# Optimization experiments

Hardware: AMD Instinct MI355X
Metric: run time of the kernel (lower is better)

## Reference

```python
import jax, jax.numpy as jnp
import numpy as np

D = 4096  # uniform layer width (sizes[i])
L = 4     # number of MyLinear layers (maximum)


def setup_inputs() -> dict:
    key = jax.random.key(0)
    ks = jax.random.split(key, 8)
    x = jax.random.normal(ks[0], (D,), jnp.float32)
    W_in = jax.random.normal(ks[1], (D, D), jnp.float32) / np.float32(np.sqrt(D))
    b_in = jax.random.normal(ks[2], (D,), jnp.float32) * 0.01
    weights = jax.random.normal(ks[3], (L, D, D), jnp.float32) / np.float32(np.sqrt(D))
    # `order` is a fixed 0/1-style connectivity mask (requires_grad=False in torch)
    orders = (jax.random.uniform(ks[4], (L, D, D)) < 0.5).astype(jnp.float32)
    biases = jax.random.normal(ks[5], (L, D), jnp.float32) * 0.01
    # input_layer[i]: which node slots feed layer i (irregular gather)
    gather_idx = jax.random.randint(ks[6], (L, D), 0, D)
    # layer_nodes[k]: where layer outputs are scattered (per-layer permutation)
    scatter_idx = jnp.stack(
        [jax.random.permutation(jax.random.fold_in(ks[7], i), D) for i in range(L + 1)]
    )
    return dict(x=x, W_in=W_in, b_in=b_in, weights=weights, orders=orders,
                biases=biases, gather_idx=gather_idx, scatter_idx=scatter_idx)


def reference(x, W_in, b_in, weights, orders, biases, gather_idx, scatter_idx):
    # input layer: relu(Linear(x)), scattered into the node buffer
    out0 = jax.nn.relu(W_in @ x + b_in)              # [D]
    buf = jnp.zeros_like(out0).at[scatter_idx[0]].set(out0)

    def step(buf, layer):
        W, O, b, g, s = layer
        inp = buf[g]                                  # gather node values [D]
        out = jax.nn.relu((W * O) @ inp + b)          # masked GEMV + bias + relu
        new_buf = jnp.zeros_like(out).at[s].set(out)  # scatter into node buffer
        return new_buf, out

    _, outs = jax.lax.scan(
        step, buf, (weights, orders, biases, gather_idx, scatter_idx[1:])
    )
    return outs[-1]  # forward returns the last layer's (pre-scatter) output
```

## Files before the change

kernel.cpp:

```cpp
#include <hip/hip_runtime.h>
#include <hip/hip_bf16.h>


#define DD 4096
#define BLOCK 512
#define GRID  512

template<bool MASKED>
__global__ __launch_bounds__(BLOCK)
void gemv_kernel(const float* __restrict__ W,
                 const float* __restrict__ O,
                 const float* __restrict__ bias,
                 const float* __restrict__ src,
                 const int*   __restrict__ g,
                 const int*   __restrict__ s,
                 float*       __restrict__ dst)
{
    __shared__ float sh[DD];
    const int tid = threadIdx.x;

    #pragma unroll
    for (int j = tid; j < DD; j += BLOCK)
        sh[j] = MASKED ? src[g[j]] : src[j];
    __syncthreads();

    const int lane = tid & 63;
    const int wv   = tid >> 6;
    const int row  = blockIdx.x * 8 + wv;

    const float* __restrict__ Wr = W + (size_t)row * DD + lane * 4;
    const float* __restrict__ Or = MASKED ? (O + (size_t)row * DD + lane * 4)
                                          : nullptr;

    float4 w[16];
    #pragma unroll
    for (int it = 0; it < 16; ++it)
        w[it] = *reinterpret_cast<const float4*>(Wr + it * 256);

    float4 o[16];
    if (MASKED) {
        #pragma unroll
        for (int it = 0; it < 16; ++it)
            o[it] = *reinterpret_cast<const float4*>(Or + it * 256);
    }

    float a0 = 0.f, a1 = 0.f, a2 = 0.f, a3 = 0.f;
    #pragma unroll
    for (int it = 0; it < 16; ++it) {
        float4 v = *reinterpret_cast<const float4*>(sh + it * 256 + lane * 4);
        float4 ww = w[it];
        if (MASKED) {
            ww.x *= o[it].x; ww.y *= o[it].y; ww.z *= o[it].z; ww.w *= o[it].w;
        }
        a0 = fmaf(ww.x, v.x, a0);
        a1 = fmaf(ww.y, v.y, a1);
        a2 = fmaf(ww.z, v.z, a2);
        a3 = fmaf(ww.w, v.w, a3);
    }
    float acc = (a0 + a1) + (a2 + a3);

    #pragma unroll
    for (int off = 32; off > 0; off >>= 1)
        acc += __shfl_xor(acc, off, 64);

    if (lane == 0) {
        float r = fmaxf(acc + bias[row], 0.f);
        if (s) dst[s[row]] = r;
        else   dst[row]    = r;
    }
}

extern "C" void kernel_launch(void* const* d_in, const int* in_sizes, int n_in,
                              void* d_out, int out_size, void* d_ws, size_t ws_size,
                              hipStream_t stream) {
    const float* x       = (const float*)d_in[0];
    const float* W_in    = (const float*)d_in[1];
    const float* b_in    = (const float*)d_in[2];
    const float* weights = (const float*)d_in[3];
    const float* orders  = (const float*)d_in[4];
    const float* biases  = (const float*)d_in[5];
    const int*   gidx    = (const int*)d_in[6];
    const int*   sidx    = (const int*)d_in[7];
    float*       out     = (float*)d_out;

    float* buf0 = (float*)d_ws;
    float* buf1 = buf0 + DD;

    gemv_kernel<false><<<GRID, BLOCK, 0, stream>>>(
        W_in, nullptr, b_in, x, nullptr, sidx, buf0);

    float* cur = buf0;
    float* nxt = buf1;
    for (int l = 0; l < 4; ++l) {
        const int* s  = (l == 3) ? nullptr : (sidx + (size_t)(l + 1) * DD);
        float*     d  = (l == 3) ? out     : nxt;
        gemv_kernel<true><<<GRID, BLOCK, 0, stream>>>(
            weights + (size_t)l * DD * DD,
            orders  + (size_t)l * DD * DD,
            biases  + (size_t)l * DD,
            cur, gidx + (size_t)l * DD, s, d);
        float* t = cur; cur = nxt; nxt = t;
    }
}
```

Baseline: 558.6 us.

## Fuse all five GEMV layers into one persistent kernel with grid barriers

Replaces five separate kernel launches with a single persistent kernel of 256 blocks × 1024 threads that runs the input layer and all four masked layers, with atomic-counter grid barriers between layers. This removes per-launch overhead and the gaps between dependent kernels. It adds a memset of the barrier counters, relies on all 256 blocks being co-resident (not guaranteed by a cooperative launch), and no longer prefetches all weight and mask loads into registers before the dot product.

```diff
diff --git a/kernel.cpp b/kernel.cpp
--- a/kernel.cpp
+++ b/kernel.cpp
@@ -3,70 +3,92 @@
 
 
 #define DD 4096
-#define BLOCK 512
-#define GRID  512
+#define NB 256
+#define NT 1024
+#define NLAYER 4
 
-template<bool MASKED>
-__global__ __launch_bounds__(BLOCK)
-void gemv_kernel(const float* __restrict__ W,
-                 const float* __restrict__ O,
-                 const float* __restrict__ bias,
-                 const float* __restrict__ src,
-                 const int*   __restrict__ g,
-                 const int*   __restrict__ s,
-                 float*       __restrict__ dst)
+__device__ __forceinline__ void grid_barrier(int* cnt) {
+    __syncthreads();
+    if (threadIdx.x == 0) {
+        __threadfence();
+        __hip_atomic_fetch_add(cnt, 1, __ATOMIC_ACQ_REL, __HIP_MEMORY_SCOPE_AGENT);
+        while (__hip_atomic_load(cnt, __ATOMIC_ACQUIRE, __HIP_MEMORY_SCOPE_AGENT) < NB) {}
+        __threadfence();
+    }
+    __syncthreads();
+}
+
+__global__ __launch_bounds__(NT, 4)
+void fused_net(const float* __restrict__ x,
+               const float* __restrict__ W_in,
+               const float* __restrict__ b_in,
+               const float* __restrict__ weights,
+               const float* __restrict__ orders,
+               const float* __restrict__ biases,
+               const int*   __restrict__ gidx,
+               const int*   __restrict__ sidx,
+               float*       __restrict__ out,
+               float*       __restrict__ buf0,
+               float*       __restrict__ buf1,
+               int*         __restrict__ cnt)
 {
     __shared__ float sh[DD];
-    const int tid = threadIdx.x;
-
-    #pragma unroll
-    for (int j = tid; j < DD; j += BLOCK)
-        sh[j] = MASKED ? src[g[j]] : src[j];
-    __syncthreads();
-
+    const int tid  = threadIdx.x;
     const int lane = tid & 63;
     const int wv   = tid >> 6;
-    const int row  = blockIdx.x * 8 + wv;
+    const int row  = blockIdx.x * 16 + wv;
 
-    const float* __restrict__ Wr = W + (size_t)row * DD + lane * 4;
-    const float* __restrict__ Or = MASKED ? (O + (size_t)row * DD + lane * 4)
-                                          : nullptr;
+    for (int j = tid; j < DD; j += NT) sh[j] = x[j];
+    __syncthreads();
+    {
+        const float* Wr = W_in + (size_t)row * DD + lane * 4;
+        float a0 = 0.f, a1 = 0.f, a2 = 0.f, a3 = 0.f;
+        #pragma unroll
+        for (int it = 0; it < 16; ++it) {
+            float4 w = *reinterpret_cast<const float4*>(Wr + it * 256);
+            float4 v = *reinterpret_cast<const float4*>(sh + it * 256 + lane * 4);
+            a0 = fmaf(w.x, v.x, a0); a1 = fmaf(w.y, v.y, a1);
+            a2 = fmaf(w.z, v.z, a2); a3 = fmaf(w.w, v.w, a3);
+        }
+        float acc = (a0 + a1) + (a2 + a3);
+        #pragma unroll
+        for (int off = 32; off; off >>= 1) acc += __shfl_xor(acc, off, 64);
+        if (lane == 0) buf0[sidx[row]] = fmaxf(acc + b_in[row], 0.f);
+    }
+    grid_barrier(cnt + 0);
 
-    float4 w[16];
+    float* bufs[2] = { buf0, buf1 };
     #pragma unroll
-    for (int it = 0; it < 16; ++it)
-        w[it] = *reinterpret_cast<const float4*>(Wr + it * 256);
+    for (int l = 0; l < NLAYER; ++l) {
+        const float* src = bufs[l & 1];
+        const int*   g   = gidx + (size_t)l * DD;
+        for (int j = tid; j < DD; j += NT) sh[j] = src[g[j]];
+        __syncthreads();
 
-    float4 o[16];
-    if (MASKED) {
+        const float* Wr = weights + (size_t)l * DD * DD + (size_t)row * DD + lane * 4;
+        const float* Or = orders  + (size_t)l * DD * DD + (size_t)row * DD + lane * 4;
+        float a0 = 0.f, a1 = 0.f, a2 = 0.f, a3 = 0.f;
         #pragma unroll
-        for (int it = 0; it < 16; ++it)
-            o[it] = *reinterpret_cast<const float4*>(Or + it * 256);
-    }
+        for (int it = 0; it < 16; ++it) {
+            float4 w = *reinterpret_cast<const float4*>(Wr + it * 256);
+            float4 o = *reinterpret_cast<const float4*>(Or + it * 256);
+            float4 v = *reinterpret_cast<const float4*>(sh + it * 256 + lane * 4);
+            a0 = fmaf(w.x * o.x, v.x, a0);
+            a1 = fmaf(w.y * o.y, v.y, a1);
+            a2 = fmaf(w.z * o.z, v.z, a2);
+            a3 = fmaf(w.w * o.w, v.w, a3);
+        }
+        float acc = (a0 + a1) + (a2 + a3);
+        #pragma unroll
+        for (int off = 32; off; off >>= 1) acc += __shfl_xor(acc, off, 64);
+        float r = fmaxf(acc + biases[(size_t)l * DD + row], 0.f);
 
-    float a0 = 0.f, a1 = 0.f, a2 = 0.f, a3 = 0.f;
-    #pragma unroll
-    for (int it = 0; it < 16; ++it) {
-        float4 v = *reinterpret_cast<const float4*>(sh + it * 256 + lane * 4);
-        float4 ww = w[it];
-        if (MASKED) {
-            ww.x *= o[it].x; ww.y *= o[it].y; ww.z *= o[it].z; ww.w *= o[it].w;
+        if (l == NLAYER - 1) {
+            if (lane == 0) out[row] = r;
+        } else {
+            if (lane == 0) bufs[(l + 1) & 1][sidx[(size_t)(l + 1) * DD + row]] = r;
+            grid_barrier(cnt + 1 + l);
         }
-        a0 = fmaf(ww.x, v.x, a0);
-        a1 = fmaf(ww.y, v.y, a1);
-        a2 = fmaf(ww.z, v.z, a2);
-        a3 = fmaf(ww.w, v.w, a3);
-    }
-    float acc = (a0 + a1) + (a2 + a3);
-
-    #pragma unroll
-    for (int off = 32; off > 0; off >>= 1)
-        acc += __shfl_xor(acc, off, 64);
-
-    if (lane == 0) {
-        float r = fmaxf(acc + bias[row], 0.f);
-        if (s) dst[s[row]] = r;
-        else   dst[row]    = r;
     }
 }
 
@@ -83,22 +105,12 @@
     const int*   sidx    = (const int*)d_in[7];
     float*       out     = (float*)d_out;
 
-    float* buf0 = (float*)d_ws;
+    int*   cnt  = (int*)d_ws;
+    float* buf0 = (float*)((char*)d_ws + 256);
     float* buf1 = buf0 + DD;
 
-    gemv_kernel<false><<<GRID, BLOCK, 0, stream>>>(
-        W_in, nullptr, b_in, x, nullptr, sidx, buf0);
+    hipMemsetAsync(d_ws, 0, 256, stream);
 
-    float* cur = buf0;
-    float* nxt = buf1;
-    for (int l = 0; l < 4; ++l) {
-        const int* s  = (l == 3) ? nullptr : (sidx + (size_t)(l + 1) * DD);
-        float*     d  = (l == 3) ? out     : nxt;
-        gemv_kernel<true><<<GRID, BLOCK, 0, stream>>>(
-            weights + (size_t)l * DD * DD,
-            orders  + (size_t)l * DD * DD,
-            biases  + (size_t)l * DD,
-            cur, gidx + (size_t)l * DD, s, d);
-        float* t = cur; cur = nxt; nxt = t;
-    }
+    fused_net<<<NB, NT, 0, stream>>>(x, W_in, b_in, weights, orders, biases,
+                                     gidx, sidx, out, buf0, buf1, cnt);
 }
```

New measurement: 660.4 us. 18.2% more time.

## Issue weight loads before gather barrier and double-buffer with larger blocks

Applied to the files above, without the earlier changes.

The weight and mask row loads now start before the shared-memory gather and __syncthreads, so HBM traffic overlaps the gather latency. Register buffers are halved to 8 float4 each, and the second half of the row is loaded into slots freed during the first half of the compute loop. Blocks grow to 1024 threads (16 rows per block) with a 4-waves-per-EU launch bound, halving the grid. This cuts register pressure and raises the number of loads in flight, at the cost of bigger blocks whose barrier waits on more waves.

```diff
diff --git a/kernel.cpp b/kernel.cpp
--- a/kernel.cpp
+++ b/kernel.cpp
@@ -3,11 +3,11 @@
 
 
 #define DD 4096
-#define BLOCK 512
-#define GRID  512
+#define BLOCK 1024
+#define GRID  256
 
 template<bool MASKED>
-__global__ __launch_bounds__(BLOCK)
+__global__ __launch_bounds__(BLOCK, 4)
 void gemv_kernel(const float* __restrict__ W,
                  const float* __restrict__ O,
                  const float* __restrict__ bias,
@@ -17,51 +17,48 @@
                  float*       __restrict__ dst)
 {
     __shared__ float sh[DD];
-    const int tid = threadIdx.x;
+    const int tid  = threadIdx.x;
+    const int lane = tid & 63;
+    const int wv   = tid >> 6;
+    const int row  = blockIdx.x * 16 + wv;
+
+    const float* __restrict__ Wr = W + (size_t)row * DD + lane * 4;
+    const float* __restrict__ Or = MASKED ? (O + (size_t)row * DD + lane * 4)
+                                          : nullptr;
+
+    float4 wb[8], ob[8];
+    #pragma unroll
+    for (int k = 0; k < 8; ++k) {
+        wb[k] = *reinterpret_cast<const float4*>(Wr + k * 256);
+        if (MASKED) ob[k] = *reinterpret_cast<const float4*>(Or + k * 256);
+    }
 
     #pragma unroll
     for (int j = tid; j < DD; j += BLOCK)
         sh[j] = MASKED ? src[g[j]] : src[j];
     __syncthreads();
 
-    const int lane = tid & 63;
-    const int wv   = tid >> 6;
-    const int row  = blockIdx.x * 8 + wv;
-
-    const float* __restrict__ Wr = W + (size_t)row * DD + lane * 4;
-    const float* __restrict__ Or = MASKED ? (O + (size_t)row * DD + lane * 4)
-                                          : nullptr;
-
-    float4 w[16];
-    #pragma unroll
-    for (int it = 0; it < 16; ++it)
-        w[it] = *reinterpret_cast<const float4*>(Wr + it * 256);
-
-    float4 o[16];
-    if (MASKED) {
-        #pragma unroll
-        for (int it = 0; it < 16; ++it)
-            o[it] = *reinterpret_cast<const float4*>(Or + it * 256);
-    }
-
     float a0 = 0.f, a1 = 0.f, a2 = 0.f, a3 = 0.f;
     #pragma unroll
     for (int it = 0; it < 16; ++it) {
         float4 v = *reinterpret_cast<const float4*>(sh + it * 256 + lane * 4);
-        float4 ww = w[it];
-        if (MASKED) {
-            ww.x *= o[it].x; ww.y *= o[it].y; ww.z *= o[it].z; ww.w *= o[it].w;
+        float4 w = wb[it & 7];
+        float4 o;
+        if (MASKED) o = ob[it & 7];
+        if (it < 8) {
+            wb[it] = *reinterpret_cast<const float4*>(Wr + (it + 8) * 256);
+            if (MASKED) ob[it] = *reinterpret_cast<const float4*>(Or + (it + 8) * 256);
         }
-        a0 = fmaf(ww.x, v.x, a0);
-        a1 = fmaf(ww.y, v.y, a1);
-        a2 = fmaf(ww.z, v.z, a2);
-        a3 = fmaf(ww.w, v.w, a3);
+        if (MASKED) { w.x *= o.x; w.y *= o.y; w.z *= o.z; w.w *= o.w; }
+        a0 = fmaf(w.x, v.x, a0);
+        a1 = fmaf(w.y, v.y, a1);
+        a2 = fmaf(w.z, v.z, a2);
+        a3 = fmaf(w.w, v.w, a3);
     }
     float acc = (a0 + a1) + (a2 + a3);
 
     #pragma unroll
-    for (int off = 32; off > 0; off >>= 1)
-        acc += __shfl_xor(acc, off, 64);
+    for (int off = 32; off; off >>= 1) acc += __shfl_xor(acc, off, 64);
 
     if (lane == 0) {
         float r = fmaxf(acc + bias[row], 0.f);
```

After: 548.5 us. Within noise of the previous version (-1.8%).
